# Performance work log

Measured on AMD Instinct MI355X. Metric: run time of the kernel, lower is better.

The kernel has to match this reference:

```python
import jax, jax.numpy as jnp
import numpy as np

T_STEPS = 4
K = 16
TAU = 2.0      # spikingjelly LIFNode default tau
VTH = 1.0      # default v_threshold, v_reset=0, hard reset, decay_input=True
EPS = 1e-5
ALPHA = 2.0    # ATan surrogate default

@jax.custom_vjp
def spike(x):
    return (x >= 0.0).astype(x.dtype)

def _spike_fwd(x):
    return spike(x), x

def _spike_bwd(x, g):
    return (g * (ALPHA / 2.0) / (1.0 + (jnp.pi / 2.0 * ALPHA * x) ** 2),)

spike.defvjp(_spike_fwd, _spike_bwd)

def lif(x_seq):
    # multi-step LIF over leading time axis, v0=0
    def step(v, x):
        v = v + (x - v) / TAU          # decay_input=True, v_reset=0
        s = spike(v - VTH)
        return v * (1.0 - s), s        # hard reset to 0
    _, s_seq = jax.lax.scan(step, jnp.zeros_like(x_seq[0]), x_seq)
    return s_seq

def bntt(x, gamma, beta):
    # per-timestep BatchNorm (training-mode batch stats), x: [T,B,C,...]
    red = (1,) + tuple(range(3, x.ndim))
    mean = x.mean(axis=red, keepdims=True)
    var = ((x - mean) ** 2).mean(axis=red, keepdims=True)
    shp = (x.shape[0], 1, x.shape[2]) + (1,) * (x.ndim - 3)
    return (x - mean) * jax.lax.rsqrt(var + EPS) * gamma.reshape(shp) + beta.reshape(shp)

def graph_feature(x, k):
    # x: [B,C,N]; kNN on first 3 channels, DGCNN edge features [B,2C,N,k]
    pos = x[:, :3]
    inner = jnp.einsum('bcn,bcm->bnm', pos, pos)
    sq = jnp.sum(pos ** 2, axis=1)                     # [B,N]
    neg_d = 2.0 * inner - sq[:, :, None] - sq[:, None, :]
    idx = jax.lax.top_k(neg_d, k)[1]                   # [B,N,k]
    xt = jnp.swapaxes(x, 1, 2)                         # [B,N,C]
    nbr = jax.vmap(lambda f, i: f[i])(xt, idx)         # [B,N,k,C]
    ctr = xt[:, :, None, :]
    feat = jnp.concatenate([jnp.broadcast_to(ctr, nbr.shape), nbr - ctr], axis=-1)
    return jnp.transpose(feat, (0, 3, 1, 2))           # [B,2C,N,k]

def _forward(x, t_w1, t_b1, t_w2, t_b2, t_w3, t_b3, t_fw1, t_fb1, t_fw2, t_fb2,
             t_fw3, t_fb3, w1, w2, w3, w4, g1, be1, g2, be2, g3, be3, g4, be4):
    pos = x[:, :3]                                       # [B,3,N]
    # --- SpikingTNet ---
    xs = jnp.broadcast_to(pos[None], (T_STEPS,) + pos.shape)
    h = lif(jnp.einsum('tbcn,dc->tbdn', xs, t_w1) + t_b1[:, None])
    h = lif(jnp.einsum('tbcn,dc->tbdn', h, t_w2) + t_b2[:, None])
    h = lif(jnp.einsum('tbcn,dc->tbdn', h, t_w3) + t_b3[:, None])
    h = h.max(axis=3)                                    # [T,B,1024]
    h = lif(h @ t_fw1.T + t_fb1)
    h = lif(h @ t_fw2.T + t_fb2)
    h = h @ t_fw3.T + t_fb3                              # [T,B,9]
    trans = h.mean(axis=0).reshape(-1, 3, 3) + jnp.eye(3, dtype=x.dtype)
    # --- align + graph feature ---
    pos_a = jnp.einsum('bcn,bcd->bdn', pos, trans)
    xa = jnp.concatenate([pos_a, x[:, 3:]], axis=1)      # [B,14,N]
    gfeat = graph_feature(xa, K)                         # [B,28,N,K]
    gs = jnp.broadcast_to(gfeat[None], (T_STEPS,) + gfeat.shape)
    # --- spiking encoder ---
    h = lif(bntt(jnp.einsum('tbcnk,dc->tbdnk', gs, w1), g1, be1))
    h = lif(bntt(jnp.einsum('tbcnk,dc->tbdnk', h, w2), g2, be2))
    h = h.max(axis=4)                                    # [T,B,128,N]
    h = lif(bntt(jnp.einsum('tbcn,dc->tbdn', h, w3), g3, be3))
    h = lif(bntt(jnp.einsum('tbcn,dc->tbdn', h, w4), g4, be4))
    return h.max(axis=3).mean(axis=0)                    # [B,1024]

def setup_inputs():
    key = jax.random.key(0)
    ks = jax.random.split(key, 16)
    def w(i, shape, fan):
        return jax.random.normal(ks[i], shape, dtype=jnp.float32) / np.sqrt(fan)
    B, N = 8, 2048
    z = lambda *s: jnp.zeros(s, jnp.float32)
    o = lambda *s: jnp.ones(s, jnp.float32)
    return {
        'x': jax.random.normal(ks[0], (B, 14, N), dtype=jnp.float32),
        't_w1': w(1, (64, 3), 3), 't_b1': z(64),
        't_w2': w(2, (128, 64), 64), 't_b2': z(128),
        't_w3': w(3, (1024, 128), 128), 't_b3': z(1024),
        't_fw1': w(4, (512, 1024), 1024), 't_fb1': z(512),
        't_fw2': w(5, (256, 512), 512), 't_fb2': z(256),
        't_fw3': w(6, (9, 256), 256), 't_fb3': z(9),
        'w1': w(7, (64, 28), 28),
        'w2': w(8, (128, 64), 64),
        'w3': w(9, (256, 128), 128),
        'w4': w(10, (1024, 256), 256),
        'g1': o(T_STEPS, 64), 'be1': z(T_STEPS, 64),
        'g2': o(T_STEPS, 128), 'be2': z(T_STEPS, 128),
        'g3': o(T_STEPS, 256), 'be3': z(T_STEPS, 256),
        'g4': o(T_STEPS, 1024), 'be4': z(T_STEPS, 1024),
    }

def reference(x, t_w1, t_b1, t_w2, t_b2, t_w3, t_b3, t_fw1, t_fb1, t_fw2, t_fb2,
              t_fw3, t_fb3, w1, w2, w3, w4, g1, be1, g2, be2, g3, be3, g4, be4):
    return _forward(x, t_w1, t_b1, t_w2, t_b2, t_w3, t_b3, t_fw1, t_fb1, t_fw2,
                    t_fb2, t_fw3, t_fb3, w1, w2, w3, w4, g1, be1, g2, be2, g3,
                    be3, g4, be4)
```

## Files before the change

### kernel.cpp

```cpp
#include <hip/hip_runtime.h>
#include <stdint.h>

#define TT 4
#define BB 8
#define NN 2048
#define KNB 16
#define PP (NN*KNB)
#define VTH 1.0f
#define EPSB 1e-5f

typedef unsigned long long u64;
typedef unsigned int u32;
typedef unsigned short u16;
typedef unsigned char u8;
typedef __attribute__((ext_vector_type(8))) short short8;
typedef __attribute__((ext_vector_type(4))) float f4;

#define GLOAD_LDS16(g, l) __builtin_amdgcn_global_load_lds( \
    (const __attribute__((address_space(1))) u32*)(g), \
    (__attribute__((address_space(3))) u32*)(l), 16, 0, 0)

__device__ __forceinline__ float lif_step(float& v, float x) {
    v = v + (x - v) / 2.0f;
    float s = (v - VTH >= 0.0f) ? 1.0f : 0.0f;
    v = v * (1.0f - s);
    return s;
}

__global__ __launch_bounds__(256) void k_tnet1(const float* __restrict__ x, const float* __restrict__ w,
        const float* __restrict__ bi, u64* __restrict__ s1b) {
    int i = blockIdx.x*256 + threadIdx.x;
    int b = i >> 11, n = i & 2047;
    float p0 = x[((size_t)b*14+0)*NN+n];
    float p1 = x[((size_t)b*14+1)*NN+n];
    float p2 = x[((size_t)b*14+2)*NN+n];
    u64 m[TT] = {0,0,0,0};
    for (int d = 0; d < 64; ++d) {
        float z = ((w[d*3+0]*p0 + w[d*3+1]*p1) + w[d*3+2]*p2) + bi[d];
        float v = 0.f;
        #pragma unroll
        for (int t = 0; t < TT; ++t) {
            float s = lif_step(v, z);
            if (s != 0.f) m[t] |= (1ull << d);
        }
    }
    #pragma unroll
    for (int t = 0; t < TT; ++t) s1b[((size_t)t*BB + b)*NN + n] = m[t];
}

__global__ __launch_bounds__(256) void k_tnet2(const u64* __restrict__ s1b, const float* __restrict__ w,
        const float* __restrict__ bi, u32* __restrict__ s2b32) {
    __shared__ float ws[32*64];
    int tid = threadIdx.x;
    int ec = blockIdx.y;
    for (int l = tid; l < 32*64; l += 256) ws[l] = w[ec*32*64 + l];
    __syncthreads();
    int i = blockIdx.x*256 + tid;
    int b = i >> 11, n = i & 2047;
    u64 m[TT];
    #pragma unroll
    for (int t = 0; t < TT; ++t) m[t] = s1b[((size_t)t*BB+b)*NN+n];
    u32 o[TT] = {0,0,0,0};
    for (int el = 0; el < 32; ++el) {
        float z[TT] = {0.f,0.f,0.f,0.f};
        #pragma unroll 8
        for (int d = 0; d < 64; ++d) {
            float wv = ws[el*64+d];
            #pragma unroll
            for (int t = 0; t < TT; ++t) z[t] += ((m[t]>>d)&1ull) ? wv : 0.f;
        }
        float v = 0.f, bb = bi[ec*32 + el];
        #pragma unroll
        for (int t = 0; t < TT; ++t) {
            float s = lif_step(v, z[t] + bb);
            if (s != 0.f) o[t] |= (1u << el);
        }
    }
    #pragma unroll
    for (int t = 0; t < TT; ++t)
        s2b32[(((size_t)t*BB+b)*NN+n)*4 + ec] = o[t];
}

__global__ __launch_bounds__(64) void k_fc1(const u32* __restrict__ mx, const float* __restrict__ fw1,
        const float* __restrict__ fb1, float* __restrict__ h1v) {
    int f = blockIdx.x, b = blockIdx.y, lane = threadIdx.x;
    float wr[16];
    #pragma unroll
    for (int j = 0; j < 16; ++j) wr[j] = fw1[(size_t)f*1024 + j*64 + lane];
    float z[TT];
    #pragma unroll
    for (int t = 0; t < TT; ++t) {
        float s = 0.f;
        #pragma unroll
        for (int j = 0; j < 16; ++j)
            s += wr[j] * (float)mx[((size_t)t*BB+b)*1024 + j*64 + lane];
        #pragma unroll
        for (int o = 1; o < 64; o <<= 1) s += __shfl_xor(s, o, 64);
        z[t] = s;
    }
    if (lane == 0) {
        float v = 0.f;
        #pragma unroll
        for (int t = 0; t < TT; ++t)
            h1v[((size_t)t*BB+b)*512 + f] = lif_step(v, z[t] + fb1[f]);
    }
}

__global__ __launch_bounds__(64) void k_fc2(const float* __restrict__ h1v, const float* __restrict__ fw2,
        const float* __restrict__ fb2, float* __restrict__ h2v) {
    int f = blockIdx.x, b = blockIdx.y, lane = threadIdx.x;
    float wr[8];
    #pragma unroll
    for (int j = 0; j < 8; ++j) wr[j] = fw2[(size_t)f*512 + j*64 + lane];
    float z[TT];
    #pragma unroll
    for (int t = 0; t < TT; ++t) {
        float s = 0.f;
        #pragma unroll
        for (int j = 0; j < 8; ++j)
            s += wr[j] * h1v[((size_t)t*BB+b)*512 + j*64 + lane];
        #pragma unroll
        for (int o = 1; o < 64; o <<= 1) s += __shfl_xor(s, o, 64);
        z[t] = s;
    }
    if (lane == 0) {
        float v = 0.f;
        #pragma unroll
        for (int t = 0; t < TT; ++t)
            h2v[((size_t)t*BB+b)*256 + f] = lif_step(v, z[t] + fb2[f]);
    }
}

__global__ __launch_bounds__(64) void k_fc3(const float* __restrict__ h2v, const float* __restrict__ fw3,
        const float* __restrict__ fb3, float* __restrict__ trans) {
    __shared__ float h3s[TT][9];
    int b = blockIdx.x, tid = threadIdx.x;
    if (tid < TT*9) {
        int t = tid/9, oo = tid%9;
        float z = 0.f;
        for (int c = 0; c < 256; ++c) z += fw3[oo*256+c]*h2v[((size_t)t*BB+b)*256 + c];
        h3s[t][oo] = z + fb3[oo];
    }
    __syncthreads();
    if (tid < 9) {
        float m = ((h3s[0][tid]+h3s[1][tid]) + (h3s[2][tid]+h3s[3][tid])) * 0.25f;
        int c = tid/3, dd = tid%3;
        trans[b*9+tid] = m + ((c==dd)?1.0f:0.0f);
    }
}

__global__ __launch_bounds__(256) void k_trans(const float* __restrict__ x, const float* __restrict__ tr,
        float* __restrict__ xa, float4* __restrict__ xa4) {
    int i = blockIdx.x*256 + threadIdx.x;
    int b = i >> 11, n = i & 2047;
    float p0 = x[((size_t)b*14+0)*NN+n];
    float p1 = x[((size_t)b*14+1)*NN+n];
    float p2 = x[((size_t)b*14+2)*NN+n];
    const float* tb = tr + b*9;
    float a0 = (p0*tb[0] + p1*tb[3]) + p2*tb[6];
    float a1 = (p0*tb[1] + p1*tb[4]) + p2*tb[7];
    float a2 = (p0*tb[2] + p1*tb[5]) + p2*tb[8];
    xa[((size_t)b*14+0)*NN+n] = a0;
    xa[((size_t)b*14+1)*NN+n] = a1;
    xa[((size_t)b*14+2)*NN+n] = a2;
    for (int c = 3; c < 14; ++c) xa[((size_t)b*14+c)*NN+n] = x[((size_t)b*14+c)*NN+n];
    float4 p;
    p.x = a0; p.y = a1; p.z = a2;
    p.w = (a0*a0 + a1*a1) + a2*a2;
    xa4[(size_t)b*NN+n] = p;
}

__global__ __launch_bounds__(256) void k_knn(const float4* __restrict__ xa4, int* __restrict__ idx) {
    int wave = threadIdx.x >> 6, lane = threadIdx.x & 63;
    int b = blockIdx.y;
    int n = blockIdx.x*4 + wave;
    const float4* P = xa4 + (size_t)b*NN;
    float4 q = P[n];
    float sn = q.w;
    float vals[32];
    #pragma unroll
    for (int j = 0; j < 32; ++j) {
        float4 p = P[j*64 + lane];
        float inner = (q.x*p.x + q.y*p.y) + q.z*p.z;
        vals[j] = (2.0f*inner - sn) - p.w;
    }
    for (int k = 0; k < KNB; ++k) {
        float bv = -3.4e38f; int bj = 0;
        #pragma unroll
        for (int j = 0; j < 32; ++j) if (vals[j] > bv) { bv = vals[j]; bj = j; }
        int bm = bj*64 + lane;
        u32 fb = __float_as_uint(bv);
        fb = (fb & 0x80000000u) ? ~fb : (fb | 0x80000000u);
        u64 key = ((u64)fb << 32) | (u32)(~bm);
        #pragma unroll
        for (int o2 = 1; o2 < 64; o2 <<= 1) {
            u64 other = __shfl_xor(key, o2, 64);
            key = (other > key) ? other : key;
        }
        int wm = (int)(~(u32)key);
        if (lane == 0) idx[((size_t)b*NN + n)*KNB + k] = wm;
        int wl = wm & 63, wj = wm >> 6;
        if (lane == wl) {
            #pragma unroll
            for (int j = 0; j < 32; ++j) if (j == wj) vals[j] = -3.4e38f;
        }
    }
}

__global__ __launch_bounds__(256) void k_gfeat(const float* __restrict__ xa, const int* __restrict__ idx, float* __restrict__ gf) {
    int i = blockIdx.x*256 + threadIdx.x;
    int b = i >> 15;
    int r = i & 32767;
    int n = r >> 4;
    int mm = idx[((size_t)b*NN+n)*KNB + (r & 15)];
    size_t pbase = (size_t)b*28*PP + r;
    #pragma unroll
    for (int c = 0; c < 14; ++c) {
        float ctr = xa[((size_t)b*14+c)*NN + n];
        float nb  = xa[((size_t)b*14+c)*NN + mm];
        gf[pbase + (size_t)c*PP] = ctr;
        gf[pbase + (size_t)(14+c)*PP] = nb - ctr;
    }
}

__global__ __launch_bounds__(256) void k_estats1(const float* __restrict__ gf, const float* __restrict__ w1, float* __restrict__ part1) {
    __shared__ float gfs[28][256];
    __shared__ float w1s[64*28];
    __shared__ float wsum[4][64], wsq[4][64];
    int pt = blockIdx.x, b = blockIdx.y;
    int p0 = pt*256, tid = threadIdx.x;
    for (int l = tid; l < 28*256; l += 256) gfs[l>>8][l&255] = gf[((size_t)b*28 + (l>>8))*PP + p0 + (l&255)];
    for (int l = tid; l < 64*28; l += 256) w1s[l] = w1[l];
    __syncthreads();
    int wv = tid>>6, lane = tid&63;
    for (int d = 0; d < 64; ++d) {
        float z = 0.f;
        #pragma unroll
        for (int c = 0; c < 28; ++c) z += w1s[d*28+c]*gfs[c][tid];
        float s = z, q = z*z;
        #pragma unroll
        for (int o = 1; o < 64; o <<= 1) { s += __shfl_xor(s, o, 64); q += __shfl_xor(q, o, 64); }
        if (lane == 0) { wsum[wv][d] = s; wsq[wv][d] = q; }
    }
    __syncthreads();
    if (tid < 64) {
        float s = (wsum[0][tid]+wsum[1][tid])+(wsum[2][tid]+wsum[3][tid]);
        float q = (wsq[0][tid]+wsq[1][tid])+(wsq[2][tid]+wsq[3][tid]);
        size_t blk = (size_t)b*128 + pt;
        part1[(blk*64 + tid)*2+0] = s;
        part1[(blk*64 + tid)*2+1] = q;
    }
}

__global__ __launch_bounds__(256) void k_reduce(const float* __restrict__ part, float* __restrict__ stats, int nch, int nblk, double M) {
    __shared__ double sred[256], qred[256];
    int ch = blockIdx.x, tid = threadIdx.x;
    double s = 0.0, q = 0.0;
    for (int i = tid; i < nblk; i += 256) {
        s += (double)part[((size_t)i*nch + ch)*2 + 0];
        q += (double)part[((size_t)i*nch + ch)*2 + 1];
    }
    sred[tid] = s; qred[tid] = q;
    __syncthreads();
    for (int off = 128; off > 0; off >>= 1) {
        if (tid < off) { sred[tid] += sred[tid+off]; qred[tid] += qred[tid+off]; }
        __syncthreads();
    }
    if (tid == 0) {
        double mu = sred[0] / M;
        double var = qred[0] / M - mu*mu;
        if (var < 0.0) var = 0.0;
        stats[ch*2+0] = (float)mu;
        stats[ch*2+1] = 1.0f / sqrtf((float)var + EPSB);
    }
}

__global__ __launch_bounds__(256) void k_h1(const float* __restrict__ gf, const float* __restrict__ w1,
        const float* __restrict__ st1, const float* __restrict__ g1, const float* __restrict__ be1,
        u64* __restrict__ h1b, u64* __restrict__ h1n) {
    __shared__ float w1s[64*28];
    int tid = threadIdx.x;
    int b = blockIdx.y;
    int p0 = blockIdx.x*256;
    int p = p0 + tid;
    for (int l = tid; l < 64*28; l += 256) w1s[l] = w1[l];
    __syncthreads();
    float gr[28];
    #pragma unroll
    for (int c = 0; c < 28; ++c) gr[c] = gf[((size_t)b*28 + c)*PP + p];
    int wordbase = (p0>>6) + (tid>>6);
    u64 pm[TT] = {0,0,0,0};
    for (int d = 0; d < 64; ++d) {
        float z = 0.f;
        #pragma unroll
        for (int c = 0; c < 28; ++c) z += w1s[d*28+c]*gr[c];
        float mu = st1[d*2+0], iv = st1[d*2+1];
        float v = 0.f;
        #pragma unroll
        for (int t = 0; t < TT; ++t) {
            float y = (z - mu) * iv * g1[t*64+d] + be1[t*64+d];
            float s = lif_step(v, y);
            u64 m = __ballot(s != 0.f);
            if ((tid & 63) == 0) h1b[((size_t)(t*BB+b)*64 + d)*512 + wordbase] = m;
            pm[t] |= ((u64)(s != 0.f)) << d;
        }
    }
    #pragma unroll
    for (int t = 0; t < TT; ++t) h1n[(size_t)(t*BB+b)*PP + p] = pm[t];
}

__global__ __launch_bounds__(256) void k_gram_h1(const u64* __restrict__ h1b, int* __restrict__ Mi) {
    __shared__ u64 tw[64*65];
    int tid = threadIdx.x;
    int w0 = blockIdx.x*64;
    int tb = blockIdx.y;
    int t = tb >> 3;
    const u64* src = h1b + (size_t)tb*64*512;
    for (int l = tid; l < 64*64; l += 256) {
        int c = l >> 6, w = l & 63;
        tw[c*65+w] = src[(size_t)c*512 + w0 + w];
    }
    __syncthreads();
    int q = tid >> 4, r = tid & 15;
    int acc[4][4];
    #pragma unroll
    for (int i=0;i<4;++i)
        #pragma unroll
        for (int j=0;j<4;++j) acc[i][j]=0;
    #pragma unroll 4
    for (int w = 0; w < 64; ++w) {
        u64 av[4], bv[4];
        #pragma unroll
        for (int i=0;i<4;++i) av[i] = tw[(q+16*i)*65+w];
        #pragma unroll
        for (int j=0;j<4;++j) bv[j] = tw[(r+16*j)*65+w];
        #pragma unroll
        for (int i=0;i<4;++i)
            #pragma unroll
            for (int j=0;j<4;++j) acc[i][j] += (int)__popcll(av[i]&bv[j]);
    }
    #pragma unroll
    for (int i=0;i<4;++i)
        #pragma unroll
        for (int j=0;j<4;++j)
            atomicAdd(&Mi[((size_t)t*64 + q+16*i)*64 + r+16*j], acc[i][j]);
}

template<int C>
__global__ __launch_bounds__(256) void k_gram2(const u64* __restrict__ bits, int* __restrict__ Mi) {
    __shared__ u64 ta[64*33], tbt[64*33];
    int tid = threadIdx.x;
    int ci0 = blockIdx.x*64, cj0 = blockIdx.y*64;
    int tb = blockIdx.z;
    int t = tb >> 3;
    const u64* srcA = bits + ((size_t)tb*C + ci0)*32;
    const u64* srcB = bits + ((size_t)tb*C + cj0)*32;
    for (int l = tid; l < 64*32; l += 256) {
        int rr = l >> 5, w = l & 31;
        ta[rr*33+w]  = srcA[(size_t)rr*32+w];
        tbt[rr*33+w] = srcB[(size_t)rr*32+w];
    }
    __syncthreads();
    int q = tid >> 4, r = tid & 15;
    int acc[4][4];
    #pragma unroll
    for (int i=0;i<4;++i)
        #pragma unroll
        for (int j=0;j<4;++j) acc[i][j]=0;
    #pragma unroll 4
    for (int w = 0; w < 32; ++w) {
        u64 av[4], bv[4];
        #pragma unroll
        for (int i=0;i<4;++i) av[i] = ta[(q+16*i)*33+w];
        #pragma unroll
        for (int j=0;j<4;++j) bv[j] = tbt[(r+16*j)*33+w];
        #pragma unroll
        for (int i=0;i<4;++i)
            #pragma unroll
            for (int j=0;j<4;++j) acc[i][j] += (int)__popcll(av[i]&bv[j]);
    }
    #pragma unroll
    for (int i=0;i<4;++i)
        #pragma unroll
        for (int j=0;j<4;++j)
            atomicAdd(&Mi[((size_t)t*C + ci0+q+16*i)*C + cj0+r+16*j], acc[i][j]);
}

template<int CIN>
__global__ void k_proj(const int* __restrict__ Mf, const float* __restrict__ w,
        float* __restrict__ st, int COUT, double cnt) {
    __shared__ double z2s[256], mns[256];
    int ch = blockIdx.x, t = blockIdx.y, c2 = threadIdx.x;
    const int* Mt = Mf + (size_t)t*CIN*CIN;
    double y = 0.0;
    for (int c = 0; c < CIN; ++c)
        y += (double)w[(size_t)ch*CIN+c] * (double)Mt[(size_t)c*CIN + c2];
    double wc2 = (double)w[(size_t)ch*CIN+c2];
    z2s[c2] = wc2 * y;
    mns[c2] = wc2 * (double)Mt[(size_t)c2*CIN + c2];
    __syncthreads();
    for (int off = CIN>>1; off > 0; off >>= 1) {
        if (c2 < off) { z2s[c2] += z2s[c2+off]; mns[c2] += mns[c2+off]; }
        __syncthreads();
    }
    if (c2 == 0) {
        double mu = mns[0] / cnt;
        double var = z2s[0] / cnt - mu*mu;
        if (var < 0.0) var = 0.0;
        st[((size_t)t*COUT+ch)*2+0] = (float)mu;
        st[((size_t)t*COUT+ch)*2+1] = 1.0f / sqrtf((float)var + EPSB);
    }
}

__global__ __launch_bounds__(256) void k_wprep(const float* __restrict__ w,
        short* __restrict__ hi, short* __restrict__ mid, short* __restrict__ lo, int F, int K) {
    int i = blockIdx.x*256 + threadIdx.x;
    if (i >= F*K) return;
    int f = i / K, k = i % K;
    float wv = w[i];
    u32 b0 = __float_as_uint(wv);
    float h = __uint_as_float(b0 & 0xFFFF0000u);
    float r1 = wv - h;
    u32 b1 = __float_as_uint(r1);
    float m = __uint_as_float(b1 & 0xFFFF0000u);
    float r2 = r1 - m;
    u32 b2 = __float_as_uint(r2);
    size_t o = ((size_t)(k>>3)*F + f)*8 + (k&7);
    hi[o]  = (short)(b0 >> 16);
    mid[o] = (short)(b1 >> 16);
    lo[o]  = (short)(b2 >> 16);
}

template<int K, int F, int MODE, bool BITS>
__global__ __launch_bounds__(256) void k_mconv(
        const void* __restrict__ Asrc,
        const short* __restrict__ Whi, const short* __restrict__ Wmd, const short* __restrict__ Wlo,
        const float* __restrict__ st, const float* __restrict__ ga, const float* __restrict__ be,
        const float* __restrict__ bias,
        u16* __restrict__ outp, u32* __restrict__ outm, int NPTS) {
    constexpr int KT = 64;
    constexpr int ROWS = (KT/8)*3;
    constexpr int NW = (K+63)/64;
    __shared__ short wsm[ROWS*512];
    __shared__ short sptab[BITS ? 256*8 : 8];
    __shared__ u32 morr[TT][64];
    int tid = threadIdx.x;
    int wave = tid >> 6, lane = tid & 63;
    int l15 = lane & 15, lg = lane >> 4;
    int b = blockIdx.z;
    int n_base = blockIdx.x*64 + wave*16;
    int f0 = blockIdx.y*64;
    if (MODE == 0 || MODE == 2)
        for (int l = tid; l < TT*64; l += 256) morr[l>>6][l&63] = 0u;
    if (BITS) {
        #pragma unroll
        for (int j = 0; j < 8; ++j) sptab[tid*8+j] = (short)(((tid>>j)&1) * 0x3F80);
    }

    f4 acc[4][TT];
    #pragma unroll
    for (int i = 0; i < 4; ++i)
        #pragma unroll
        for (int t = 0; t < TT; ++t) acc[i][t] = (f4)0.f;

    u64 aw[TT][NW];
    const u16* Au[TT];
    #pragma unroll
    for (int t = 0; t < TT; ++t) {
        if (BITS) {
            const u64* Ab = (const u64*)Asrc + ((size_t)(t*BB+b)*NPTS + n_base + l15)*NW;
            #pragma unroll
            for (int wq = 0; wq < NW; ++wq) aw[t][wq] = Ab[wq];
        } else {
            Au[t] = (const u16*)Asrc + ((size_t)(t*BB+b)*NPTS + n_base + l15)*K + lg*8;
        }
    }
    const short* Wsrc[3] = {Whi, Wmd, Wlo};

    #pragma unroll
    for (int kt = 0; kt < K; kt += KT) {
        if (kt > 0) __syncthreads();
        #pragma unroll
        for (int r = wave; r < ROWS; r += 4) {
            int kq = r/3, s = r - kq*3;
            const short* g = Wsrc[s] + ((size_t)((kt>>3) + kq)*F + f0)*8 + lane*8;
            GLOAD_LDS16(g, &wsm[r*512]);
        }
        __syncthreads();
        #pragma unroll
        for (int k0 = 0; k0 < KT; k0 += 32) {
            int kg = kt + k0;
            short8 a[TT];
            #pragma unroll
            for (int t = 0; t < TT; ++t) {
                if (BITS) {
                    u32 byte = (u32)(aw[t][kg>>6] >> ((kg&63) + lg*8)) & 0xFFu;
                    a[t] = *(const short8*)(sptab + byte*8);
                } else {
                    a[t] = *(const short8*)(Au[t] + kg);
                }
            }
            int kql = (k0>>3) + lg;
            #pragma unroll
            for (int fs = 0; fs < 4; ++fs) {
                const short* base = wsm + kql*1536 + (fs*16+l15)*8;
                short8 whi = *(const short8*)(base);
                short8 wmd = *(const short8*)(base + 512);
                short8 wlo = *(const short8*)(base + 1024);
                #pragma unroll
                for (int t = 0; t < TT; ++t) {
                    acc[fs][t] = __builtin_amdgcn_mfma_f32_16x16x32_bf16(a[t], whi, acc[fs][t], 0, 0, 0);
                    acc[fs][t] = __builtin_amdgcn_mfma_f32_16x16x32_bf16(a[t], wmd, acc[fs][t], 0, 0, 0);
                    acc[fs][t] = __builtin_amdgcn_mfma_f32_16x16x32_bf16(a[t], wlo, acc[fs][t], 0, 0, 0);
                }
            }
        }
    }
    if (MODE == 1) {
        #pragma unroll
        for (int fs = 0; fs < 4; ++fs) {
            int f = f0 + fs*16 + l15;
            #pragma unroll
            for (int reg = 0; reg < 4; ++reg) {
                int n = n_base + lg*4 + reg;
                float v = 0.f;
                #pragma unroll
                for (int t = 0; t < TT; ++t) {
                    int ch = t*F + f;
                    float y = (acc[fs][t][reg] - st[(size_t)ch*2+0])*st[(size_t)ch*2+1]*ga[ch] + be[ch];
                    float s = lif_step(v, y);
                    outp[((size_t)(t*BB+b)*NPTS + n)*F + f] = (s != 0.f) ? (u16)0x3F80 : (u16)0;
                }
            }
        }
    } else if (MODE == 3) {
        #pragma unroll
        for (int fs = 0; fs < 4; ++fs) {
            int f = f0 + fs*16 + l15;
            u32 nib = 0u;
            #pragma unroll
            for (int reg = 0; reg < 4; ++reg) {
                float v = 0.f;
                #pragma unroll
                for (int t = 0; t < TT; ++t) {
                    int ch = t*F + f;
                    float y = (acc[fs][t][reg] - st[(size_t)ch*2+0])*st[(size_t)ch*2+1]*ga[ch] + be[ch];
                    float s = lif_step(v, y);
                    if (s != 0.f) nib |= (1u << t);
                }
            }
            nib |= __shfl_xor(nib, 16, 64);
            nib |= __shfl_xor(nib, 32, 64);
            if (lg == 0) {
                int n_pt = n_base >> 4;
                #pragma unroll
                for (int t = 0; t < TT; ++t)
                    outp[((size_t)(t*BB+b)*(NPTS>>4) + n_pt)*F + f] = ((nib>>t)&1u) ? (u16)0x3F80 : (u16)0;
            }
        }
    } else {
        #pragma unroll
        for (int fs = 0; fs < 4; ++fs) {
            int f = f0 + fs*16 + l15;
            u32 any[TT] = {0,0,0,0};
            float bb = (MODE == 0) ? bias[f] : 0.f;
            #pragma unroll
            for (int reg = 0; reg < 4; ++reg) {
                float v = 0.f;
                #pragma unroll
                for (int t = 0; t < TT; ++t) {
                    float y;
                    if (MODE == 0) y = acc[fs][t][reg] + bb;
                    else {
                        int ch = t*F + f;
                        y = (acc[fs][t][reg] - st[(size_t)ch*2+0])*st[(size_t)ch*2+1]*ga[ch] + be[ch];
                    }
                    float s = lif_step(v, y);
                    if (s != 0.f) any[t] = 1u;
                }
            }
            #pragma unroll
            for (int t = 0; t < TT; ++t) if (any[t]) atomicOr(&morr[t][fs*16+l15], 1u);
        }
        __syncthreads();
        for (int l = tid; l < TT*64; l += 256)
            if (morr[l>>6][l&63]) atomicOr(&outm[((size_t)((l>>6)*BB+b))*F + f0 + (l&63)], 1u);
    }
}

template<int C>
__global__ __launch_bounds__(256) void k_repack(const u16* __restrict__ sp, u64* __restrict__ bits) {
    __shared__ u16 tile[64][C+2];
    int tid = threadIdx.x;
    int nw = blockIdx.x, b = blockIdx.y, t = blockIdx.z;
    const u16* src = sp + ((size_t)(t*BB+b)*NN + nw*64)*C;
    for (int i = tid*2; i < 64*C; i += 512) {
        u32 v = *(const u32*)(src + i);
        int r = i / C, c = i % C;
        *(u32*)&tile[r][c] = v;
    }
    __syncthreads();
    int wave = tid >> 6, lane = tid & 63;
    for (int c = wave; c < C; c += 4) {
        u64 m = __ballot(tile[lane][c] != 0);
        if (lane == 0) bits[((size_t)(t*BB+b)*C + c)*32 + nw] = m;
    }
}

__global__ __launch_bounds__(256) void k_out(const u32* __restrict__ mx4, float* __restrict__ out) {
    int i = blockIdx.x*256 + threadIdx.x;
    int b = i >> 10, g = i & 1023;
    float s = (float)(mx4[((size_t)0*BB+b)*1024+g] + mx4[((size_t)1*BB+b)*1024+g]
                    + mx4[((size_t)2*BB+b)*1024+g] + mx4[((size_t)3*BB+b)*1024+g]);
    out[i] = s * 0.25f;
}

extern "C" void kernel_launch(void* const* d_in, const int* in_sizes, int n_in,
                              void* d_out, int out_size, void* d_ws, size_t ws_size,
                              hipStream_t stream) {
    (void)in_sizes; (void)n_in; (void)out_size;
    const float* x    = (const float*)d_in[0];
    const float* tw1  = (const float*)d_in[1];
    const float* tb1  = (const float*)d_in[2];
    const float* tw2  = (const float*)d_in[3];
    const float* tb2  = (const float*)d_in[4];
    const float* tw3  = (const float*)d_in[5];
    const float* tb3  = (const float*)d_in[6];
    const float* tfw1 = (const float*)d_in[7];
    const float* tfb1 = (const float*)d_in[8];
    const float* tfw2 = (const float*)d_in[9];
    const float* tfb2 = (const float*)d_in[10];
    const float* tfw3 = (const float*)d_in[11];
    const float* tfb3 = (const float*)d_in[12];
    const float* w1   = (const float*)d_in[13];
    const float* w2   = (const float*)d_in[14];
    const float* w3   = (const float*)d_in[15];
    const float* w4   = (const float*)d_in[16];
    const float* g1   = (const float*)d_in[17];
    const float* be1  = (const float*)d_in[18];
    const float* g2   = (const float*)d_in[19];
    const float* be2  = (const float*)d_in[20];
    const float* g3   = (const float*)d_in[21];
    const float* be3  = (const float*)d_in[22];
    const float* g4   = (const float*)d_in[23];
    const float* be4  = (const float*)d_in[24];

    char* wsb = (char*)d_ws;
    size_t off = 0;
    auto alloc = [&](size_t bytes) -> void* {
        void* p = wsb + off;
        off = (off + bytes + 255) & ~(size_t)255;
        return p;
    };
    u64* s1b   = (u64*)alloc(sizeof(u64)*(size_t)TT*BB*NN);
    u64* s2b   = (u64*)alloc(sizeof(u64)*(size_t)TT*BB*NN*2);
    u32* mx    = (u32*)alloc(sizeof(u32)*(size_t)TT*BB*1024);
    u32* mx4   = (u32*)alloc(sizeof(u32)*(size_t)TT*BB*1024);
    float* trs = (float*)alloc(sizeof(float)*BB*9);
    float* xa  = (float*)alloc(sizeof(float)*(size_t)BB*14*NN);
    float4* xa4 = (float4*)alloc(sizeof(float4)*(size_t)BB*NN);
    int* idx   = (int*)alloc(sizeof(int)*(size_t)BB*NN*KNB);
    float* gf  = (float*)alloc(sizeof(float)*(size_t)BB*28*PP);
    float* part1 = (float*)alloc(sizeof(float)*(size_t)1024*64*2);
    float* st1 = (float*)alloc(sizeof(float)*64*2);
    float* st2 = (float*)alloc(sizeof(float)*512*2);
    float* st3 = (float*)alloc(sizeof(float)*1024*2);
    float* st4 = (float*)alloc(sizeof(float)*4096*2);
    float* h1v = (float*)alloc(sizeof(float)*(size_t)TT*BB*512);
    float* h2v = (float*)alloc(sizeof(float)*(size_t)TT*BB*256);
    u64* h1b = (u64*)alloc(sizeof(u64)*(size_t)TT*BB*64*512);
    u64* h1n = (u64*)alloc(sizeof(u64)*(size_t)TT*BB*PP);
    u16* m2p = (u16*)alloc(sizeof(u16)*(size_t)TT*BB*NN*128);
    u16* h3p = (u16*)alloc(sizeof(u16)*(size_t)TT*BB*NN*256);
    u64* m2b = (u64*)alloc(sizeof(u64)*(size_t)TT*BB*128*32);
    u64* h3b = (u64*)alloc(sizeof(u64)*(size_t)TT*BB*256*32);
    int* Mi64  = (int*)alloc(sizeof(int)*(size_t)TT*64*64);
    int* Mi128 = (int*)alloc(sizeof(int)*(size_t)TT*128*128);
    int* Mi256 = (int*)alloc(sizeof(int)*(size_t)TT*256*256);
    short* wp2h = (short*)alloc(sizeof(short)*(size_t)128*64);
    short* wp2m = (short*)alloc(sizeof(short)*(size_t)128*64);
    short* wp2l = (short*)alloc(sizeof(short)*(size_t)128*64);
    short* wp3h = (short*)alloc(sizeof(short)*(size_t)256*128);
    short* wp3m = (short*)alloc(sizeof(short)*(size_t)256*128);
    short* wp3l = (short*)alloc(sizeof(short)*(size_t)256*128);
    short* wp4h = (short*)alloc(sizeof(short)*(size_t)1024*256);
    short* wp4m = (short*)alloc(sizeof(short)*(size_t)1024*256);
    short* wp4l = (short*)alloc(sizeof(short)*(size_t)1024*256);
    short* wpth = (short*)alloc(sizeof(short)*(size_t)1024*128);
    short* wptm = (short*)alloc(sizeof(short)*(size_t)1024*128);
    short* wptl = (short*)alloc(sizeof(short)*(size_t)1024*128);
    if (off > ws_size) return;

    hipMemsetAsync(mx, 0, sizeof(u32)*(size_t)TT*BB*1024, stream);
    hipMemsetAsync(mx4, 0, sizeof(u32)*(size_t)TT*BB*1024, stream);
    hipMemsetAsync(Mi64, 0, sizeof(int)*(size_t)TT*64*64, stream);
    hipMemsetAsync(Mi128, 0, sizeof(int)*(size_t)TT*128*128, stream);
    hipMemsetAsync(Mi256, 0, sizeof(int)*(size_t)TT*256*256, stream);

    k_wprep<<<dim3((128*64+255)/256), dim3(256), 0, stream>>>(w2, wp2h, wp2m, wp2l, 128, 64);
    k_wprep<<<dim3((256*128+255)/256), dim3(256), 0, stream>>>(w3, wp3h, wp3m, wp3l, 256, 128);
    k_wprep<<<dim3((1024*256+255)/256), dim3(256), 0, stream>>>(w4, wp4h, wp4m, wp4l, 1024, 256);
    k_wprep<<<dim3((1024*128+255)/256), dim3(256), 0, stream>>>(tw3, wpth, wptm, wptl, 1024, 128);

    k_tnet1<<<dim3(64), dim3(256), 0, stream>>>(x, tw1, tb1, s1b);
    k_tnet2<<<dim3(64, 4), dim3(256), 0, stream>>>(s1b, tw2, tb2, (u32*)s2b);
    k_mconv<128,1024,0,true><<<dim3(32,16,8), dim3(256), 0, stream>>>(
        s2b, wpth, wptm, wptl, nullptr, nullptr, nullptr, tb3, nullptr, mx, NN);
    k_fc1<<<dim3(512, 8), dim3(64), 0, stream>>>(mx, tfw1, tfb1, h1v);
    k_fc2<<<dim3(256, 8), dim3(64), 0, stream>>>(h1v, tfw2, tfb2, h2v);
    k_fc3<<<dim3(8), dim3(64), 0, stream>>>(h2v, tfw3, tfb3, trs);
    k_trans<<<dim3(64), dim3(256), 0, stream>>>(x, trs, xa, xa4);
    k_knn<<<dim3(NN/4, BB), dim3(256), 0, stream>>>(xa4, idx);
    k_gfeat<<<dim3((BB*NN*KNB)/256), dim3(256), 0, stream>>>(xa, idx, gf);
    k_estats1<<<dim3(128, 8), dim3(256), 0, stream>>>(gf, w1, part1);
    k_reduce<<<dim3(64), dim3(256), 0, stream>>>(part1, st1, 64, 1024, 262144.0);
    k_h1<<<dim3(128, 8), dim3(256), 0, stream>>>(gf, w1, st1, g1, be1, h1b, h1n);
    k_gram_h1<<<dim3(8, TT*BB), dim3(256), 0, stream>>>(h1b, Mi64);
    k_proj<64><<<dim3(128, TT), dim3(64), 0, stream>>>(Mi64, w2, st2, 128, 262144.0);
    k_mconv<64,128,3,true><<<dim3(PP/64,2,8), dim3(256), 0, stream>>>(
        h1n, wp2h, wp2m, wp2l, st2, g2, be2, nullptr, m2p, nullptr, PP);
    k_repack<128><<<dim3(32,8,4), dim3(256), 0, stream>>>(m2p, m2b);
    k_gram2<128><<<dim3(2,2,TT*BB), dim3(256), 0, stream>>>(m2b, Mi128);
    k_proj<128><<<dim3(256, TT), dim3(128), 0, stream>>>(Mi128, w3, st3, 256, 16384.0);
    k_mconv<128,256,1,false><<<dim3(32,4,8), dim3(256), 0, stream>>>(
        m2p, wp3h, wp3m, wp3l, st3, g3, be3, nullptr, h3p, nullptr, NN);
    k_repack<256><<<dim3(32,8,4), dim3(256), 0, stream>>>(h3p, h3b);
    k_gram2<256><<<dim3(4,4,TT*BB), dim3(256), 0, stream>>>(h3b, Mi256);
    k_proj<256><<<dim3(1024, TT), dim3(256), 0, stream>>>(Mi256, w4, st4, 1024, 16384.0);
    k_mconv<256,1024,2,false><<<dim3(32,16,8), dim3(256), 0, stream>>>(
        h3p, wp4h, wp4m, wp4l, st4, g4, be4, nullptr, nullptr, mx4, NN);
    k_out<<<dim3(32), dim3(256), 0, stream>>>(mx4, (float*)d_out);
}
```

Baseline: 730.7 us.

## Fuse edge-feature gather into stats kernel and cache first-layer conv output

```diff
diff --git a/kernel.cpp b/kernel.cpp
--- a/kernel.cpp
+++ b/kernel.cpp
@@ -207,36 +207,31 @@
     }
 }
 
-__global__ __launch_bounds__(256) void k_gfeat(const float* __restrict__ xa, const int* __restrict__ idx, float* __restrict__ gf) {
-    int i = blockIdx.x*256 + threadIdx.x;
-    int b = i >> 15;
-    int r = i & 32767;
-    int n = r >> 4;
-    int mm = idx[((size_t)b*NN+n)*KNB + (r & 15)];
-    size_t pbase = (size_t)b*28*PP + r;
-    #pragma unroll
-    for (int c = 0; c < 14; ++c) {
-        float ctr = xa[((size_t)b*14+c)*NN + n];
-        float nb  = xa[((size_t)b*14+c)*NN + mm];
-        gf[pbase + (size_t)c*PP] = ctr;
-        gf[pbase + (size_t)(14+c)*PP] = nb - ctr;
-    }
-}
-
-__global__ __launch_bounds__(256) void k_estats1(const float* __restrict__ gf, const float* __restrict__ w1, float* __restrict__ part1) {
-    __shared__ float gfs[28][256];
+__global__ __launch_bounds__(256) void k_zstats(const float* __restrict__ xa, const int* __restrict__ idx,
+        const float* __restrict__ w1, float* __restrict__ part1, float* __restrict__ z1) {
     __shared__ float w1s[64*28];
     __shared__ float wsum[4][64], wsq[4][64];
     int pt = blockIdx.x, b = blockIdx.y;
     int p0 = pt*256, tid = threadIdx.x;
-    for (int l = tid; l < 28*256; l += 256) gfs[l>>8][l&255] = gf[((size_t)b*28 + (l>>8))*PP + p0 + (l&255)];
+    int p = p0 + tid;
     for (int l = tid; l < 64*28; l += 256) w1s[l] = w1[l];
     __syncthreads();
+    int n = p >> 4;
+    int mm = idx[((size_t)b*NN+n)*KNB + (p & 15)];
+    float gr[28];
+    #pragma unroll
+    for (int c = 0; c < 14; ++c) {
+        float ctr = xa[((size_t)b*14+c)*NN + n];
+        float nb  = xa[((size_t)b*14+c)*NN + mm];
+        gr[c] = ctr;
+        gr[14+c] = nb - ctr;
+    }
     int wv = tid>>6, lane = tid&63;
     for (int d = 0; d < 64; ++d) {
         float z = 0.f;
         #pragma unroll
-        for (int c = 0; c < 28; ++c) z += w1s[d*28+c]*gfs[c][tid];
+        for (int c = 0; c < 28; ++c) z += w1s[d*28+c]*gr[c];
+        z1[((size_t)b*64+d)*PP + p] = z;
         float s = z, q = z*z;
         #pragma unroll
         for (int o = 1; o < 64; o <<= 1) { s += __shfl_xor(s, o, 64); q += __shfl_xor(q, o, 64); }
@@ -275,25 +270,17 @@
     }
 }
 
-__global__ __launch_bounds__(256) void k_h1(const float* __restrict__ gf, const float* __restrict__ w1,
+__global__ __launch_bounds__(256) void k_h1(const float* __restrict__ z1,
         const float* __restrict__ st1, const float* __restrict__ g1, const float* __restrict__ be1,
         u64* __restrict__ h1b, u64* __restrict__ h1n) {
-    __shared__ float w1s[64*28];
     int tid = threadIdx.x;
     int b = blockIdx.y;
     int p0 = blockIdx.x*256;
     int p = p0 + tid;
-    for (int l = tid; l < 64*28; l += 256) w1s[l] = w1[l];
-    __syncthreads();
-    float gr[28];
-    #pragma unroll
-    for (int c = 0; c < 28; ++c) gr[c] = gf[((size_t)b*28 + c)*PP + p];
     int wordbase = (p0>>6) + (tid>>6);
     u64 pm[TT] = {0,0,0,0};
     for (int d = 0; d < 64; ++d) {
-        float z = 0.f;
-        #pragma unroll
-        for (int c = 0; c < 28; ++c) z += w1s[d*28+c]*gr[c];
+        float z = z1[((size_t)b*64+d)*PP + p];
         float mu = st1[d*2+0], iv = st1[d*2+1];
         float v = 0.f;
         #pragma unroll
@@ -660,7 +647,7 @@
     float* xa  = (float*)alloc(sizeof(float)*(size_t)BB*14*NN);
     float4* xa4 = (float4*)alloc(sizeof(float4)*(size_t)BB*NN);
     int* idx   = (int*)alloc(sizeof(int)*(size_t)BB*NN*KNB);
-    float* gf  = (float*)alloc(sizeof(float)*(size_t)BB*28*PP);
+    float* z1  = (float*)alloc(sizeof(float)*(size_t)BB*64*PP);
     float* part1 = (float*)alloc(sizeof(float)*(size_t)1024*64*2);
     float* st1 = (float*)alloc(sizeof(float)*64*2);
     float* st2 = (float*)alloc(sizeof(float)*512*2);
@@ -711,10 +698,9 @@
     k_fc3<<<dim3(8), dim3(64), 0, stream>>>(h2v, tfw3, tfb3, trs);
     k_trans<<<dim3(64), dim3(256), 0, stream>>>(x, trs, xa, xa4);
     k_knn<<<dim3(NN/4, BB), dim3(256), 0, stream>>>(xa4, idx);
-    k_gfeat<<<dim3((BB*NN*KNB)/256), dim3(256), 0, stream>>>(xa, idx, gf);
-    k_estats1<<<dim3(128, 8), dim3(256), 0, stream>>>(gf, w1, part1);
+    k_zstats<<<dim3(128, 8), dim3(256), 0, stream>>>(xa, idx, w1, part1, z1);
     k_reduce<<<dim3(64), dim3(256), 0, stream>>>(part1, st1, 64, 1024, 262144.0);
-    k_h1<<<dim3(128, 8), dim3(256), 0, stream>>>(gf, w1, st1, g1, be1, h1b, h1n);
+    k_h1<<<dim3(128, 8), dim3(256), 0, stream>>>(z1, st1, g1, be1, h1b, h1n);
     k_gram_h1<<<dim3(8, TT*BB), dim3(256), 0, stream>>>(h1b, Mi64);
     k_proj<64><<<dim3(128, TT), dim3(64), 0, stream>>>(Mi64, w2, st2, 128, 262144.0);
     k_mconv<64,128,3,true><<<dim3(PP/64,2,8), dim3(256), 0, stream>>>(
```

After: 722.3 us. Within noise of the previous version (-1.1%).
